# Kernel optimization log

Measured on AMD Instinct MI355X. Metric: run time of the kernel, lower is better.

## Reference

```python
import jax, jax.numpy as jnp
import numpy as np

B, H, S, DK, DV = 2, 16, 2048, 64, 64


def setup_inputs() -> dict:
    key = jax.random.key(0)
    kq, kk, kv = jax.random.split(key, 3)
    Q = jax.random.normal(kq, (B, H, S, DK), dtype=jnp.float32)
    K = jax.random.normal(kk, (B, H, S, DK), dtype=jnp.float32)
    V = jax.random.normal(kv, (B, H, S, DV), dtype=jnp.float32)
    # causal mask: True = masked (upper triangle), broadcast to [B,H,S,S]
    causal = jnp.triu(jnp.ones((S, S), dtype=bool), k=1)
    attn_mask = jnp.broadcast_to(causal, (B, H, S, S))
    return {"Q": Q, "K": K, "V": V, "attn_mask": attn_mask}


def reference(Q, K, V, attn_mask):
    d_k = Q.shape[-1]
    # scores: [B,H,len_q,len_k]
    scores = jnp.einsum('bhqd,bhkd->bhqk', Q, K) / jnp.sqrt(jnp.float32(d_k))
    scores = jnp.where(attn_mask, -jnp.inf, scores)
    attn = jax.nn.softmax(scores, axis=-1)
    # context: [B,H,len_q,d_v]
    context = jnp.einsum('bhqk,bhkv->bhqv', attn, V)
    return context
```

## Files before the change

kernel.cpp:

```cpp
#include <hip/hip_runtime.h>
#include <hip/hip_bf16.h>
#include <math.h>

#define S_LEN 2048
#define DKV 64
#define NBH 32
#define QBLK 128
#define NQB (S_LEN / QBLK)
#define NKT (S_LEN / 64)
#define TILE_SH 4096

typedef __attribute__((ext_vector_type(8))) short bf16x8;
typedef __attribute__((ext_vector_type(16))) float f32x16;
typedef __attribute__((ext_vector_type(4))) float f32x4;
typedef __attribute__((ext_vector_type(4))) unsigned uint4v;

__device__ __forceinline__ short f2bf(float f) {
    union { float f; unsigned u; } x; x.f = f;
    unsigned r = (x.u + 0x7FFFu + ((x.u >> 16) & 1u)) >> 16;
    return (short)r;
}

__device__ __forceinline__ unsigned cvtpk(float lo, float hi) {
    unsigned r;
    asm("v_cvt_pk_bf16_f32 %0, %1, %2" : "=v"(r) : "v"(lo), "v"(hi));
    return r;
}

#define GLOAD_LDS16(g, s)                                                        \
    __builtin_amdgcn_global_load_lds(                                            \
        (const __attribute__((address_space(1))) unsigned*)(g),                  \
        (__attribute__((address_space(3))) unsigned*)(s), 16, 0, 0)

__global__ __launch_bounds__(256)
void prep_kv(const float* __restrict__ K, const float* __restrict__ V,
             short* __restrict__ wsK, short* __restrict__ wsV) {
    const int tile = blockIdx.x, bh = blockIdx.y, tid = threadIdx.x;
    const float* Kp = K + ((size_t)bh * S_LEN + tile * 64) * DKV;
    const float* Vp = V + ((size_t)bh * S_LEN + tile * 64) * DKV;
    short* outK = wsK + ((size_t)bh * NKT + tile) * TILE_SH;
    short* outV = wsV + ((size_t)bh * NKT + tile) * TILE_SH;

    __shared__ short Klds[64 * 64];
    __shared__ short Vl[64 * 64];

#pragma unroll
    for (int i = 0; i < 2; ++i) {
        const int chunk = i * 256 + tid;
        const int row = chunk >> 3, c8 = chunk & 7;
        const float* ksrc = Kp + row * DKV + c8 * 8;
        float4 a = *(const float4*)ksrc, b = *(const float4*)(ksrc + 4);
        uint4v tw;
        tw[0] = cvtpk(a.x, a.y); tw[1] = cvtpk(a.z, a.w);
        tw[2] = cvtpk(b.x, b.y); tw[3] = cvtpk(b.z, b.w);
        const int sidxK = (((c8 >> 1) * 2 + (row >> 5)) * 64) |
                          (((c8 & 1) << 5) | (row & 31));
        *(uint4v*)&Klds[sidxK * 8] = tw;

        const float* vs = Vp + row * DKV + c8 * 8;
        float4 c = *(const float4*)vs, d = *(const float4*)(vs + 4);
        uint4v uw;
        uw[0] = cvtpk(c.x, c.y); uw[1] = cvtpk(c.z, c.w);
        uw[2] = cvtpk(d.x, d.y); uw[3] = cvtpk(d.z, d.w);
        *(uint4v*)&Vl[chunk * 8] = uw;
    }
    __syncthreads();

#pragma unroll
    for (int i = 0; i < 2; ++i) {
        const int s = i * 256 + tid;
        *(bf16x8*)(outK + s * 8) = *(const bf16x8*)&Klds[s * 8];
        const int group = s >> 6;
        const int cc = group >> 1, th = group & 1;
        const int lane = s & 63;
        const int hh = lane >> 5, r31 = lane & 31;
        const int vd = 32 * th + r31;
        const int key0 = 16 * cc + 8 * hh;
        bf16x8 t;
#pragma unroll
        for (int j = 0; j < 8; ++j) t[j] = Vl[(key0 + j) * 64 + vd];
        *(bf16x8*)(outV + s * 8) = t;
    }
}

__global__ __launch_bounds__(256, 2)
void attn_fwd(const float* __restrict__ Q, const short* __restrict__ wsK,
              const short* __restrict__ wsV, float* __restrict__ O) {
    const int tid = threadIdx.x;
    const int l   = tid & 63;
    const int w   = tid >> 6;
    const int qc  = w & 1;
    const int ks  = w >> 1;
    const int h   = l >> 5;
    const int q31 = l & 31;

    const int id  = blockIdx.x;
    const int bh  = ((id & 7) << 2) | ((id >> 3) & 3);
    const int r5  = (id >> 5) & 7;
    const int qb  = (id < 256) ? (15 - r5) : r5;

    __shared__ char smem[65536];
    char* kstaW = smem + w * 16384;
    float* combp = (float*)smem;

    const float SCALE = 0.125f * 1.4426950408889634f;
    const float M0 = 12.0f;

    bf16x8 qf[2][4];
#pragma unroll
    for (int sp = 0; sp < 2; ++sp) {
        const int qrow = qb * QBLK + qc * 64 + sp * 32 + q31;
        const float* qr = Q + ((size_t)bh * S_LEN + qrow) * DKV;
#pragma unroll
        for (int c = 0; c < 4; ++c) {
            const int k0 = c * 16 + h * 8;
            float4 f0 = *(const float4*)(qr + k0);
            float4 f1 = *(const float4*)(qr + k0 + 4);
            bf16x8 t;
            t[0] = f2bf(f0.x * SCALE); t[1] = f2bf(f0.y * SCALE);
            t[2] = f2bf(f0.z * SCALE); t[3] = f2bf(f0.w * SCALE);
            t[4] = f2bf(f1.x * SCALE); t[5] = f2bf(f1.y * SCALE);
            t[6] = f2bf(f1.z * SCALE); t[7] = f2bf(f1.w * SCALE);
            qf[sp][c] = t;
        }
    }

    const char* gK = (const char*)(wsK + (size_t)bh * NKT * TILE_SH);
    const char* gV = (const char*)(wsV + (size_t)bh * NKT * TILE_SH);
    const int lb = l * 16;

    float lsum[2] = {0.0f, 0.0f};
    f32x16 oacc[2][2];
#pragma unroll
    for (int sp = 0; sp < 2; ++sp)
#pragma unroll
        for (int vh = 0; vh < 2; ++vh)
#pragma unroll
            for (int r = 0; r < 16; ++r) oacc[sp][vh][r] = 0.0f;

    const int tmax = 2 * qb + qc;

    if (ks <= tmax) {
        const char* kT = gK + (size_t)ks * (TILE_SH * 2);
#pragma unroll
        for (int i = 0; i < 8; ++i)
            GLOAD_LDS16(kT + i * 1024 + lb, kstaW + i * 1024);
    }

    int cur = 0;
    for (int t = ks; t <= tmax; t += 2) {
        asm volatile("s_waitcnt vmcnt(0)" ::: "memory");
        bf16x8 kf[8];
#pragma unroll
        for (int i = 0; i < 8; ++i)
            kf[i] = *(const bf16x8*)(kstaW + cur * 8192 + i * 1024 + lb);

        if (t + 2 <= tmax) {
            const char* kT2 = gK + (size_t)(t + 2) * (TILE_SH * 2);
            char* nb = kstaW + (cur ^ 1) * 8192;
#pragma unroll
            for (int i = 0; i < 8; ++i)
                GLOAD_LDS16(kT2 + i * 1024 + lb, nb + i * 1024);
        }

        const char* vT = gV + (size_t)t * (TILE_SH * 2);
        bf16x8 vf[8];
#pragma unroll
        for (int i = 0; i < 8; ++i) vf[i] = *(const bf16x8*)(vT + i * 1024 + lb);

#pragma unroll
        for (int sp = 0; sp < 2; ++sp) {
            const int qrow = qb * QBLK + qc * 64 + sp * 32 + q31;

            f32x16 sacc[2];
#pragma unroll
            for (int th = 0; th < 2; ++th)
#pragma unroll
                for (int r = 0; r < 16; ++r) sacc[th][r] = 0.0f;

            __builtin_amdgcn_s_setprio(1);
#pragma unroll
            for (int c = 0; c < 4; ++c)
#pragma unroll
                for (int th = 0; th < 2; ++th)
                    sacc[th] = __builtin_amdgcn_mfma_f32_32x32x16_bf16(
                        kf[c * 2 + th], qf[sp][c], sacc[th], 0, 0, 0);
            __builtin_amdgcn_s_setprio(0);

            if (t == tmax) {
                const int kv0 = t * 64;
#pragma unroll
                for (int th = 0; th < 2; ++th)
#pragma unroll
                    for (int r = 0; r < 16; ++r) {
                        const int key_g = kv0 + 32 * th + (r & 3) + 8 * (r >> 2) + 4 * h;
                        if (key_g > qrow) sacc[th][r] = -3.0e38f;
                    }
            }

            float rs = 0.0f;
            __builtin_amdgcn_s_setprio(1);
#pragma unroll
            for (int c = 0; c < 4; ++c) {
                const int th = c >> 1, cc = c & 1;
                float p8[8];
#pragma unroll
                for (int j = 0; j < 8; ++j) {
                    p8[j] = __builtin_amdgcn_exp2f(sacc[th][8 * cc + j] - M0);
                    rs += p8[j];
                }
                const unsigned W00 = cvtpk(p8[0], p8[1]);
                const unsigned W01 = cvtpk(p8[2], p8[3]);
                const unsigned W10 = cvtpk(p8[4], p8[5]);
                const unsigned W11 = cvtpk(p8[6], p8[7]);
                const unsigned S0 = h ? W00 : W10;
                const unsigned S1 = h ? W01 : W11;
                const unsigned K0 = h ? W10 : W00;
                const unsigned K1 = h ? W11 : W01;
                const unsigned Y0 = __shfl_xor(S0, 32);
                const unsigned Y1 = __shfl_xor(S1, 32);
                uint4v pwv;
                pwv[0] = h ? Y0 : K0;
                pwv[1] = h ? Y1 : K1;
                pwv[2] = h ? K0 : Y0;
                pwv[3] = h ? K1 : Y1;
                const bf16x8 pa = __builtin_bit_cast(bf16x8, pwv);
#pragma unroll
                for (int vh = 0; vh < 2; ++vh)
                    oacc[sp][vh] = __builtin_amdgcn_mfma_f32_32x32x16_bf16(
                        vf[c * 2 + vh], pa, oacc[sp][vh], 0, 0, 0);
            }
            __builtin_amdgcn_s_setprio(0);

            rs += __shfl_xor(rs, 32);
            lsum[sp] += rs;
        }
        cur ^= 1;
    }

    __syncthreads();
    if (ks == 1) {
#pragma unroll
        for (int sp = 0; sp < 2; ++sp) {
            float* cp = combp + ((qc * 2 + sp) * 64 + l) * 34;
            cp[0] = lsum[sp];
#pragma unroll
            for (int vh = 0; vh < 2; ++vh)
#pragma unroll
                for (int r = 0; r < 16; ++r) cp[1 + vh * 16 + r] = oacc[sp][vh][r];
        }
    }
    __syncthreads();
    if (ks == 0) {
#pragma unroll
        for (int sp = 0; sp < 2; ++sp) {
            const float* cp = combp + ((qc * 2 + sp) * 64 + l) * 34;
            const float inv = 1.0f / (lsum[sp] + cp[0]);
            const int qrow = qb * QBLK + qc * 64 + sp * 32 + q31;
            float* Op = O + ((size_t)bh * S_LEN + qrow) * DKV;
#pragma unroll
            for (int vh = 0; vh < 2; ++vh) {
#pragma unroll
                for (int g2 = 0; g2 < 4; ++g2) {
                    f32x4 ov;
#pragma unroll
                    for (int d = 0; d < 4; ++d)
                        ov[d] = (oacc[sp][vh][4 * g2 + d] +
                                 cp[1 + vh * 16 + 4 * g2 + d]) * inv;
                    *(f32x4*)(Op + 32 * vh + 8 * g2 + 4 * h) = ov;
                }
            }
        }
    }
}

extern "C" void kernel_launch(void* const* d_in, const int* in_sizes, int n_in,
                              void* d_out, int out_size, void* d_ws, size_t ws_size,
                              hipStream_t stream) {
    const float* Q = (const float*)d_in[0];
    const float* K = (const float*)d_in[1];
    const float* V = (const float*)d_in[2];
    float* O = (float*)d_out;

    short* wsK = (short*)d_ws;
    short* wsV = wsK + (size_t)NBH * NKT * TILE_SH;

    dim3 gridp(NKT, NBH);
    prep_kv<<<gridp, 256, 0, stream>>>(K, V, wsK, wsV);
    attn_fwd<<<dim3(NQB * NBH), 256, 0, stream>>>(Q, wsK, wsV, O);
}
```

Before: 47.79 us.

## Halve query block to 64 rows and share K tiles across waves via LDS

Shrinks the query block per workgroup from 128 to 64 rows, so each wave handles one 32-row strip instead of two. Each K tile is now loaded cooperatively by a wave pair into shared LDS, with block-wide barriers each iteration. The LDS footprint is halved and launch bounds raised to 4 blocks per CU to increase occupancy and spread the causal workload over a larger grid. The cost is extra __syncthreads per tile and less reuse of each loaded K/V tile across query rows.

```diff
diff --git a/kernel.cpp b/kernel.cpp
--- a/kernel.cpp
+++ b/kernel.cpp
@@ -5,7 +5,7 @@
 #define S_LEN 2048
 #define DKV 64
 #define NBH 32
-#define QBLK 128
+#define QBLK 64
 #define NQB (S_LEN / QBLK)
 #define NKT (S_LEN / 64)
 #define TILE_SH 4096
@@ -83,33 +83,35 @@
     }
 }
 
-__global__ __launch_bounds__(256, 2)
+__global__ __launch_bounds__(256, 4)
 void attn_fwd(const float* __restrict__ Q, const short* __restrict__ wsK,
               const short* __restrict__ wsV, float* __restrict__ O) {
     const int tid = threadIdx.x;
     const int l   = tid & 63;
     const int w   = tid >> 6;
-    const int qc  = w & 1;
+    const int st  = w & 1;
     const int ks  = w >> 1;
     const int h   = l >> 5;
     const int q31 = l & 31;
 
-    const int id  = blockIdx.x;
-    const int bh  = ((id & 7) << 2) | ((id >> 3) & 3);
-    const int r5  = (id >> 5) & 7;
-    const int qb  = (id < 256) ? (15 - r5) : r5;
-
-    __shared__ char smem[65536];
-    char* kstaW = smem + w * 16384;
+    const int id = blockIdx.x;
+    const int bh = ((id & 7) << 2) | ((id >> 3) & 3);
+    const int r  = (id >> 5) & 7;
+    const int qt = id >> 8;
+    const int qb = (qt == 0) ? (31 - r) : (qt == 1) ? r
+                 : (qt == 2) ? (23 - r) : (8 + r);
+
+    __shared__ char smem[32768];
+    char* kls = smem + ks * 16384;
     float* combp = (float*)smem;
 
     const float SCALE = 0.125f * 1.4426950408889634f;
     const float M0 = 12.0f;
 
-    bf16x8 qf[2][4];
-#pragma unroll
-    for (int sp = 0; sp < 2; ++sp) {
-        const int qrow = qb * QBLK + qc * 64 + sp * 32 + q31;
+    const int qrow = qb * QBLK + st * 32 + q31;
+
+    bf16x8 qf[4];
+    {
         const float* qr = Q + ((size_t)bh * S_LEN + qrow) * DKV;
 #pragma unroll
         for (int c = 0; c < 4; ++c) {
@@ -121,7 +123,7 @@
             t[2] = f2bf(f0.z * SCALE); t[3] = f2bf(f0.w * SCALE);
             t[4] = f2bf(f1.x * SCALE); t[5] = f2bf(f1.y * SCALE);
             t[6] = f2bf(f1.z * SCALE); t[7] = f2bf(f1.w * SCALE);
-            qf[sp][c] = t;
+            qf[c] = t;
         }
     }
 
@@ -129,54 +131,50 @@
     const char* gV = (const char*)(wsV + (size_t)bh * NKT * TILE_SH);
     const int lb = l * 16;
 
-    float lsum[2] = {0.0f, 0.0f};
-    f32x16 oacc[2][2];
-#pragma unroll
-    for (int sp = 0; sp < 2; ++sp)
-#pragma unroll
-        for (int vh = 0; vh < 2; ++vh)
-#pragma unroll
-            for (int r = 0; r < 16; ++r) oacc[sp][vh][r] = 0.0f;
-
-    const int tmax = 2 * qb + qc;
-
-    if (ks <= tmax) {
-        const char* kT = gK + (size_t)ks * (TILE_SH * 2);
-#pragma unroll
-        for (int i = 0; i < 8; ++i)
-            GLOAD_LDS16(kT + i * 1024 + lb, kstaW + i * 1024);
-    }
-
+    float lsum = 0.0f;
+    f32x16 oacc[2];
+#pragma unroll
+    for (int vh = 0; vh < 2; ++vh)
+#pragma unroll
+        for (int rr = 0; rr < 16; ++rr) oacc[vh][rr] = 0.0f;
+
+    if (ks <= qb) {
+        const char* kT = gK + (size_t)ks * 8192;
+#pragma unroll
+        for (int i = 0; i < 4; ++i)
+            GLOAD_LDS16(kT + st * 4096 + i * 1024 + lb,
+                        kls + st * 4096 + i * 1024);
+    }
+
+    const int niter = qb / 2 + 1;
     int cur = 0;
-    for (int t = ks; t <= tmax; t += 2) {
+    for (int it = 0; it < niter; ++it) {
+        const int t = 2 * it + ks;
+        const bool active = (t <= qb);
+
         asm volatile("s_waitcnt vmcnt(0)" ::: "memory");
-        bf16x8 kf[8];
-#pragma unroll
-        for (int i = 0; i < 8; ++i)
-            kf[i] = *(const bf16x8*)(kstaW + cur * 8192 + i * 1024 + lb);
-
-        if (t + 2 <= tmax) {
-            const char* kT2 = gK + (size_t)(t + 2) * (TILE_SH * 2);
-            char* nb = kstaW + (cur ^ 1) * 8192;
+        __syncthreads();
+
+        if (active) {
+            bf16x8 kf[8];
 #pragma unroll
             for (int i = 0; i < 8; ++i)
-                GLOAD_LDS16(kT2 + i * 1024 + lb, nb + i * 1024);
-        }
-
-        const char* vT = gV + (size_t)t * (TILE_SH * 2);
-        bf16x8 vf[8];
-#pragma unroll
-        for (int i = 0; i < 8; ++i) vf[i] = *(const bf16x8*)(vT + i * 1024 + lb);
-
-#pragma unroll
-        for (int sp = 0; sp < 2; ++sp) {
-            const int qrow = qb * QBLK + qc * 64 + sp * 32 + q31;
+                kf[i] = *(const bf16x8*)(kls + cur * 8192 + i * 1024 + lb);
+
+            if (t + 2 <= qb) {
+                const char* kT2 = gK + (size_t)(t + 2) * 8192;
+                char* nb = kls + (cur ^ 1) * 8192;
+#pragma unroll
+                for (int i = 0; i < 4; ++i)
+                    GLOAD_LDS16(kT2 + st * 4096 + i * 1024 + lb,
+                                nb + st * 4096 + i * 1024);
+            }
 
             f32x16 sacc[2];
 #pragma unroll
             for (int th = 0; th < 2; ++th)
 #pragma unroll
-                for (int r = 0; r < 16; ++r) sacc[th][r] = 0.0f;
+                for (int rr = 0; rr < 16; ++rr) sacc[th][rr] = 0.0f;
 
             __builtin_amdgcn_s_setprio(1);
 #pragma unroll
@@ -184,17 +182,23 @@
 #pragma unroll
                 for (int th = 0; th < 2; ++th)
                     sacc[th] = __builtin_amdgcn_mfma_f32_32x32x16_bf16(
-                        kf[c * 2 + th], qf[sp][c], sacc[th], 0, 0, 0);
+                        kf[c * 2 + th], qf[c], sacc[th], 0, 0, 0);
             __builtin_amdgcn_s_setprio(0);
 
-            if (t == tmax) {
+            const char* vT = gV + (size_t)t * 8192;
+            bf16x8 vf[8];
+#pragma unroll
+            for (int i = 0; i < 8; ++i)
+                vf[i] = *(const bf16x8*)(vT + i * 1024 + lb);
+
+            if (t == qb) {
                 const int kv0 = t * 64;
 #pragma unroll
                 for (int th = 0; th < 2; ++th)
 #pragma unroll
-                    for (int r = 0; r < 16; ++r) {
-                        const int key_g = kv0 + 32 * th + (r & 3) + 8 * (r >> 2) + 4 * h;
-                        if (key_g > qrow) sacc[th][r] = -3.0e38f;
+                    for (int rr = 0; rr < 16; ++rr) {
+                        const int key_g = kv0 + 32 * th + (rr & 3) + 8 * (rr >> 2) + 4 * h;
+                        if (key_g > qrow) sacc[th][rr] = -3.0e38f;
                     }
             }
 
@@ -227,48 +231,41 @@
                 const bf16x8 pa = __builtin_bit_cast(bf16x8, pwv);
 #pragma unroll
                 for (int vh = 0; vh < 2; ++vh)
-                    oacc[sp][vh] = __builtin_amdgcn_mfma_f32_32x32x16_bf16(
-                        vf[c * 2 + vh], pa, oacc[sp][vh], 0, 0, 0);
+                    oacc[vh] = __builtin_amdgcn_mfma_f32_32x32x16_bf16(
+                        vf[c * 2 + vh], pa, oacc[vh], 0, 0, 0);
             }
             __builtin_amdgcn_s_setprio(0);
 
             rs += __shfl_xor(rs, 32);
-            lsum[sp] += rs;
+            lsum += rs;
         }
         cur ^= 1;
     }
 
     __syncthreads();
     if (ks == 1) {
-#pragma unroll
-        for (int sp = 0; sp < 2; ++sp) {
-            float* cp = combp + ((qc * 2 + sp) * 64 + l) * 34;
-            cp[0] = lsum[sp];
-#pragma unroll
-            for (int vh = 0; vh < 2; ++vh)
-#pragma unroll
-                for (int r = 0; r < 16; ++r) cp[1 + vh * 16 + r] = oacc[sp][vh][r];
-        }
+        float* cp = combp + (st * 64 + l) * 33;
+        cp[0] = lsum;
+#pragma unroll
+        for (int vh = 0; vh < 2; ++vh)
+#pragma unroll
+            for (int rr = 0; rr < 16; ++rr) cp[1 + vh * 16 + rr] = oacc[vh][rr];
     }
     __syncthreads();
     if (ks == 0) {
-#pragma unroll
-        for (int sp = 0; sp < 2; ++sp) {
-            const float* cp = combp + ((qc * 2 + sp) * 64 + l) * 34;
-            const float inv = 1.0f / (lsum[sp] + cp[0]);
-            const int qrow = qb * QBLK + qc * 64 + sp * 32 + q31;
-            float* Op = O + ((size_t)bh * S_LEN + qrow) * DKV;
-#pragma unroll
-            for (int vh = 0; vh < 2; ++vh) {
-#pragma unroll
-                for (int g2 = 0; g2 < 4; ++g2) {
-                    f32x4 ov;
-#pragma unroll
-                    for (int d = 0; d < 4; ++d)
-                        ov[d] = (oacc[sp][vh][4 * g2 + d] +
-                                 cp[1 + vh * 16 + 4 * g2 + d]) * inv;
-                    *(f32x4*)(Op + 32 * vh + 8 * g2 + 4 * h) = ov;
-                }
+        const float* cp = combp + (st * 64 + l) * 33;
+        const float inv = 1.0f / (lsum + cp[0]);
+        float* Op = O + ((size_t)bh * S_LEN + qrow) * DKV;
+#pragma unroll
+        for (int vh = 0; vh < 2; ++vh) {
+#pragma unroll
+            for (int g2 = 0; g2 < 4; ++g2) {
+                f32x4 ov;
+#pragma unroll
+                for (int d = 0; d < 4; ++d)
+                    ov[d] = (oacc[vh][4 * g2 + d] +
+                             cp[1 + vh * 16 + 4 * g2 + d]) * inv;
+                *(f32x4*)(Op + 32 * vh + 8 * g2 + 4 * h) = ov;
             }
         }
     }
```

Result: no change. 47.79 us (-0.0%).

## Fuse K/V bf16 conversion into attention kernel and drop prep pass

Applied to the files above, without the earlier changes.

Removes the separate prep_kv kernel that converted K and V to bf16 in a pre-swizzled workspace layout. The attention kernel now reads fp32 K and V straight from global memory and packs them into MFMA fragments in registers; V is gathered with per-element strided loads. This removes one launch and the workspace write and read round trip. In exchange it drops the LDS double-buffered K prefetch, doubles the bytes fetched per tile, and adds many more load and convert instructions in the inner loop.

```diff
diff --git a/kernel.cpp b/kernel.cpp
--- a/kernel.cpp
+++ b/kernel.cpp
@@ -8,7 +8,6 @@
 #define QBLK 128
 #define NQB (S_LEN / QBLK)
 #define NKT (S_LEN / 64)
-#define TILE_SH 4096
 
 typedef __attribute__((ext_vector_type(8))) short bf16x8;
 typedef __attribute__((ext_vector_type(16))) float f32x16;
@@ -27,65 +26,9 @@
     return r;
 }
 
-#define GLOAD_LDS16(g, s)                                                        \
-    __builtin_amdgcn_global_load_lds(                                            \
-        (const __attribute__((address_space(1))) unsigned*)(g),                  \
-        (__attribute__((address_space(3))) unsigned*)(s), 16, 0, 0)
-
-__global__ __launch_bounds__(256)
-void prep_kv(const float* __restrict__ K, const float* __restrict__ V,
-             short* __restrict__ wsK, short* __restrict__ wsV) {
-    const int tile = blockIdx.x, bh = blockIdx.y, tid = threadIdx.x;
-    const float* Kp = K + ((size_t)bh * S_LEN + tile * 64) * DKV;
-    const float* Vp = V + ((size_t)bh * S_LEN + tile * 64) * DKV;
-    short* outK = wsK + ((size_t)bh * NKT + tile) * TILE_SH;
-    short* outV = wsV + ((size_t)bh * NKT + tile) * TILE_SH;
-
-    __shared__ short Klds[64 * 64];
-    __shared__ short Vl[64 * 64];
-
-#pragma unroll
-    for (int i = 0; i < 2; ++i) {
-        const int chunk = i * 256 + tid;
-        const int row = chunk >> 3, c8 = chunk & 7;
-        const float* ksrc = Kp + row * DKV + c8 * 8;
-        float4 a = *(const float4*)ksrc, b = *(const float4*)(ksrc + 4);
-        uint4v tw;
-        tw[0] = cvtpk(a.x, a.y); tw[1] = cvtpk(a.z, a.w);
-        tw[2] = cvtpk(b.x, b.y); tw[3] = cvtpk(b.z, b.w);
-        const int sidxK = (((c8 >> 1) * 2 + (row >> 5)) * 64) |
-                          (((c8 & 1) << 5) | (row & 31));
-        *(uint4v*)&Klds[sidxK * 8] = tw;
-
-        const float* vs = Vp + row * DKV + c8 * 8;
-        float4 c = *(const float4*)vs, d = *(const float4*)(vs + 4);
-        uint4v uw;
-        uw[0] = cvtpk(c.x, c.y); uw[1] = cvtpk(c.z, c.w);
-        uw[2] = cvtpk(d.x, d.y); uw[3] = cvtpk(d.z, d.w);
-        *(uint4v*)&Vl[chunk * 8] = uw;
-    }
-    __syncthreads();
-
-#pragma unroll
-    for (int i = 0; i < 2; ++i) {
-        const int s = i * 256 + tid;
-        *(bf16x8*)(outK + s * 8) = *(const bf16x8*)&Klds[s * 8];
-        const int group = s >> 6;
-        const int cc = group >> 1, th = group & 1;
-        const int lane = s & 63;
-        const int hh = lane >> 5, r31 = lane & 31;
-        const int vd = 32 * th + r31;
-        const int key0 = 16 * cc + 8 * hh;
-        bf16x8 t;
-#pragma unroll
-        for (int j = 0; j < 8; ++j) t[j] = Vl[(key0 + j) * 64 + vd];
-        *(bf16x8*)(outV + s * 8) = t;
-    }
-}
-
 __global__ __launch_bounds__(256, 2)
-void attn_fwd(const float* __restrict__ Q, const short* __restrict__ wsK,
-              const short* __restrict__ wsV, float* __restrict__ O) {
+void attn_fwd(const float* __restrict__ Q, const float* __restrict__ K,
+              const float* __restrict__ V, float* __restrict__ O) {
     const int tid = threadIdx.x;
     const int l   = tid & 63;
     const int w   = tid >> 6;
@@ -99,9 +42,7 @@
     const int r5  = (id >> 5) & 7;
     const int qb  = (id < 256) ? (15 - r5) : r5;
 
-    __shared__ char smem[65536];
-    char* kstaW = smem + w * 16384;
-    float* combp = (float*)smem;
+    __shared__ float combp[2 * 2 * 64 * 34];
 
     const float SCALE = 0.125f * 1.4426950408889634f;
     const float M0 = 12.0f;
@@ -125,9 +66,8 @@
         }
     }
 
-    const char* gK = (const char*)(wsK + (size_t)bh * NKT * TILE_SH);
-    const char* gV = (const char*)(wsV + (size_t)bh * NKT * TILE_SH);
-    const int lb = l * 16;
+    const float* Kp = K + (size_t)bh * S_LEN * DKV;
+    const float* Vp = V + (size_t)bh * S_LEN * DKV;
 
     float lsum[2] = {0.0f, 0.0f};
     f32x16 oacc[2][2];
@@ -140,33 +80,50 @@
 
     const int tmax = 2 * qb + qc;
 
-    if (ks <= tmax) {
-        const char* kT = gK + (size_t)ks * (TILE_SH * 2);
-#pragma unroll
-        for (int i = 0; i < 8; ++i)
-            GLOAD_LDS16(kT + i * 1024 + lb, kstaW + i * 1024);
-    }
-
-    int cur = 0;
     for (int t = ks; t <= tmax; t += 2) {
-        asm volatile("s_waitcnt vmcnt(0)" ::: "memory");
+        const int kv0 = t * 64;
+
         bf16x8 kf[8];
 #pragma unroll
-        for (int i = 0; i < 8; ++i)
-            kf[i] = *(const bf16x8*)(kstaW + cur * 8192 + i * 1024 + lb);
-
-        if (t + 2 <= tmax) {
-            const char* kT2 = gK + (size_t)(t + 2) * (TILE_SH * 2);
-            char* nb = kstaW + (cur ^ 1) * 8192;
-#pragma unroll
-            for (int i = 0; i < 8; ++i)
-                GLOAD_LDS16(kT2 + i * 1024 + lb, nb + i * 1024);
-        }
-
-        const char* vT = gV + (size_t)t * (TILE_SH * 2);
+        for (int c = 0; c < 4; ++c) {
+#pragma unroll
+            for (int th = 0; th < 2; ++th) {
+                const float* kr = Kp + (size_t)(kv0 + 32 * th + q31) * DKV
+                                + c * 16 + h * 8;
+                float4 f0 = *(const float4*)kr;
+                float4 f1 = *(const float4*)(kr + 4);
+                uint4v wv;
+                wv[0] = cvtpk(f0.x, f0.y); wv[1] = cvtpk(f0.z, f0.w);
+                wv[2] = cvtpk(f1.x, f1.y); wv[3] = cvtpk(f1.z, f1.w);
+                kf[c * 2 + th] = __builtin_bit_cast(bf16x8, wv);
+            }
+        }
+
         bf16x8 vf[8];
 #pragma unroll
-        for (int i = 0; i < 8; ++i) vf[i] = *(const bf16x8*)(vT + i * 1024 + lb);
+        for (int half = 0; half < 2; ++half) {
+            float va[4][8];
+#pragma unroll
+            for (int fi = 0; fi < 4; ++fi) {
+                const int c  = (half * 4 + fi) >> 1;
+                const int vh = (half * 4 + fi) & 1;
+                const float* vb = Vp + (size_t)(kv0 + c * 16 + h * 8) * DKV
+                                + 32 * vh + q31;
+#pragma unroll
+                for (int j = 0; j < 8; ++j) va[fi][j] = vb[(size_t)j * DKV];
+            }
+#pragma unroll
+            for (int fi = 0; fi < 4; ++fi) {
+                const int c  = (half * 4 + fi) >> 1;
+                const int vh = (half * 4 + fi) & 1;
+                uint4v wv;
+                wv[0] = cvtpk(va[fi][0], va[fi][1]);
+                wv[1] = cvtpk(va[fi][2], va[fi][3]);
+                wv[2] = cvtpk(va[fi][4], va[fi][5]);
+                wv[3] = cvtpk(va[fi][6], va[fi][7]);
+                vf[c * 2 + vh] = __builtin_bit_cast(bf16x8, wv);
+            }
+        }
 
 #pragma unroll
         for (int sp = 0; sp < 2; ++sp) {
@@ -188,7 +145,6 @@
             __builtin_amdgcn_s_setprio(0);
 
             if (t == tmax) {
-                const int kv0 = t * 64;
 #pragma unroll
                 for (int th = 0; th < 2; ++th)
 #pragma unroll
@@ -235,10 +191,8 @@
             rs += __shfl_xor(rs, 32);
             lsum[sp] += rs;
         }
-        cur ^= 1;
-    }
-
-    __syncthreads();
+    }
+
     if (ks == 1) {
 #pragma unroll
         for (int sp = 0; sp < 2; ++sp) {
@@ -282,10 +236,5 @@
     const float* V = (const float*)d_in[2];
     float* O = (float*)d_out;
 
-    short* wsK = (short*)d_ws;
-    short* wsV = wsK + (size_t)NBH * NKT * TILE_SH;
-
-    dim3 gridp(NKT, NBH);
-    prep_kv<<<gridp, 256, 0, stream>>>(K, V, wsK, wsV);
-    attn_fwd<<<dim3(NQB * NBH), 256, 0, stream>>>(Q, wsK, wsV, O);
-}
+    attn_fwd<<<dim3(NQB * NBH), 256, 0, stream>>>(Q, K, V, O);
+}
```

Measured after the change: 78.35 us. +64.0%, slower.

## Fuse K/V bf16 prep into attention kernel with per-head atomic barrier

Applied to the files above, without the earlier changes.

Merges the separate K/V conversion kernel into the attention kernel. Each of the 512 blocks converts two K/V tiles for its head, then spins on a per-head atomic counter until all 16 blocks for that head have finished. The aim is to remove one kernel launch and the gap between the two kernels. In exchange it adds a memset launch and a spin-wait barrier, which relies on all 16 blocks of a head being co-resident and could deadlock if they are not.

```diff
diff --git a/kernel.cpp b/kernel.cpp
--- a/kernel.cpp
+++ b/kernel.cpp
@@ -32,74 +32,89 @@
         (const __attribute__((address_space(1))) unsigned*)(g),                  \
         (__attribute__((address_space(3))) unsigned*)(s), 16, 0, 0)
 
-__global__ __launch_bounds__(256)
-void prep_kv(const float* __restrict__ K, const float* __restrict__ V,
-             short* __restrict__ wsK, short* __restrict__ wsV) {
-    const int tile = blockIdx.x, bh = blockIdx.y, tid = threadIdx.x;
-    const float* Kp = K + ((size_t)bh * S_LEN + tile * 64) * DKV;
-    const float* Vp = V + ((size_t)bh * S_LEN + tile * 64) * DKV;
-    short* outK = wsK + ((size_t)bh * NKT + tile) * TILE_SH;
-    short* outV = wsV + ((size_t)bh * NKT + tile) * TILE_SH;
-
-    __shared__ short Klds[64 * 64];
-    __shared__ short Vl[64 * 64];
-
-#pragma unroll
-    for (int i = 0; i < 2; ++i) {
-        const int chunk = i * 256 + tid;
-        const int row = chunk >> 3, c8 = chunk & 7;
-        const float* ksrc = Kp + row * DKV + c8 * 8;
-        float4 a = *(const float4*)ksrc, b = *(const float4*)(ksrc + 4);
-        uint4v tw;
-        tw[0] = cvtpk(a.x, a.y); tw[1] = cvtpk(a.z, a.w);
-        tw[2] = cvtpk(b.x, b.y); tw[3] = cvtpk(b.z, b.w);
-        const int sidxK = (((c8 >> 1) * 2 + (row >> 5)) * 64) |
-                          (((c8 & 1) << 5) | (row & 31));
-        *(uint4v*)&Klds[sidxK * 8] = tw;
-
-        const float* vs = Vp + row * DKV + c8 * 8;
-        float4 c = *(const float4*)vs, d = *(const float4*)(vs + 4);
-        uint4v uw;
-        uw[0] = cvtpk(c.x, c.y); uw[1] = cvtpk(c.z, c.w);
-        uw[2] = cvtpk(d.x, d.y); uw[3] = cvtpk(d.z, d.w);
-        *(uint4v*)&Vl[chunk * 8] = uw;
+__global__ __launch_bounds__(256, 2)
+void fused_attn(const float* __restrict__ Q, const float* __restrict__ K,
+                const float* __restrict__ V, int* __restrict__ cnt,
+                short* __restrict__ wsK, short* __restrict__ wsV,
+                float* __restrict__ O) {
+    const int tid = threadIdx.x;
+    const int id  = blockIdx.x;
+    const int bh  = ((id & 7) << 2) | ((id >> 3) & 3);
+    const int jj  = id >> 5;
+
+    __shared__ char smem[65536];
+
+    {
+        short* Klds = (short*)smem;
+        short* Vl   = (short*)(smem + 8192);
+
+        for (int pp = 0; pp < 2; ++pp) {
+            const int tile = jj * 2 + pp;
+            const float* Kp = K + ((size_t)bh * S_LEN + tile * 64) * DKV;
+            const float* Vp = V + ((size_t)bh * S_LEN + tile * 64) * DKV;
+            short* outK = wsK + ((size_t)bh * NKT + tile) * TILE_SH;
+            short* outV = wsV + ((size_t)bh * NKT + tile) * TILE_SH;
+
+#pragma unroll
+            for (int i = 0; i < 2; ++i) {
+                const int chunk = i * 256 + tid;
+                const int row = chunk >> 3, c8 = chunk & 7;
+                const float* ksrc = Kp + row * DKV + c8 * 8;
+                float4 a = *(const float4*)ksrc, b = *(const float4*)(ksrc + 4);
+                uint4v tw;
+                tw[0] = cvtpk(a.x, a.y); tw[1] = cvtpk(a.z, a.w);
+                tw[2] = cvtpk(b.x, b.y); tw[3] = cvtpk(b.z, b.w);
+                const int sidxK = (((c8 >> 1) * 2 + (row >> 5)) * 64) |
+                                  (((c8 & 1) << 5) | (row & 31));
+                *(uint4v*)&Klds[sidxK * 8] = tw;
+
+                const float* vs = Vp + row * DKV + c8 * 8;
+                float4 c = *(const float4*)vs, d = *(const float4*)(vs + 4);
+                uint4v uw;
+                uw[0] = cvtpk(c.x, c.y); uw[1] = cvtpk(c.z, c.w);
+                uw[2] = cvtpk(d.x, d.y); uw[3] = cvtpk(d.z, d.w);
+                *(uint4v*)&Vl[chunk * 8] = uw;
+            }
+            __syncthreads();
+
+#pragma unroll
+            for (int i = 0; i < 2; ++i) {
+                const int s = i * 256 + tid;
+                *(bf16x8*)(outK + s * 8) = *(const bf16x8*)&Klds[s * 8];
+                const int group = s >> 6;
+                const int cc2 = group >> 1, th = group & 1;
+                const int lane = s & 63;
+                const int hh = lane >> 5, r31l = lane & 31;
+                const int vd = 32 * th + r31l;
+                const int key0 = 16 * cc2 + 8 * hh;
+                bf16x8 t;
+#pragma unroll
+                for (int j = 0; j < 8; ++j) t[j] = Vl[(key0 + j) * 64 + vd];
+                *(bf16x8*)(outV + s * 8) = t;
+            }
+            __syncthreads();
+        }
+    }
+
+    if (tid == 0) {
+        __threadfence();
+        atomicAdd(&cnt[bh], 1);
+        while (__hip_atomic_load(&cnt[bh], __ATOMIC_ACQUIRE,
+                                 __HIP_MEMORY_SCOPE_AGENT) < 16) {
+            __builtin_amdgcn_s_sleep(8);
+        }
     }
     __syncthreads();
 
-#pragma unroll
-    for (int i = 0; i < 2; ++i) {
-        const int s = i * 256 + tid;
-        *(bf16x8*)(outK + s * 8) = *(const bf16x8*)&Klds[s * 8];
-        const int group = s >> 6;
-        const int cc = group >> 1, th = group & 1;
-        const int lane = s & 63;
-        const int hh = lane >> 5, r31 = lane & 31;
-        const int vd = 32 * th + r31;
-        const int key0 = 16 * cc + 8 * hh;
-        bf16x8 t;
-#pragma unroll
-        for (int j = 0; j < 8; ++j) t[j] = Vl[(key0 + j) * 64 + vd];
-        *(bf16x8*)(outV + s * 8) = t;
-    }
-}
-
-__global__ __launch_bounds__(256, 2)
-void attn_fwd(const float* __restrict__ Q, const short* __restrict__ wsK,
-              const short* __restrict__ wsV, float* __restrict__ O) {
-    const int tid = threadIdx.x;
     const int l   = tid & 63;
     const int w   = tid >> 6;
     const int qc  = w & 1;
     const int ks  = w >> 1;
     const int h   = l >> 5;
     const int q31 = l & 31;
-
-    const int id  = blockIdx.x;
-    const int bh  = ((id & 7) << 2) | ((id >> 3) & 3);
     const int r5  = (id >> 5) & 7;
     const int qb  = (id < 256) ? (15 - r5) : r5;
 
-    __shared__ char smem[65536];
     char* kstaW = smem + w * 16384;
     float* combp = (float*)smem;
 
@@ -282,10 +297,10 @@
     const float* V = (const float*)d_in[2];
     float* O = (float*)d_out;
 
-    short* wsK = (short*)d_ws;
+    int*   cnt = (int*)d_ws;
+    short* wsK = (short*)((char*)d_ws + 1024);
     short* wsV = wsK + (size_t)NBH * NKT * TILE_SH;
 
-    dim3 gridp(NKT, NBH);
-    prep_kv<<<gridp, 256, 0, stream>>>(K, V, wsK, wsV);
-    attn_fwd<<<dim3(NQB * NBH), 256, 0, stream>>>(Q, wsK, wsV, O);
+    hipMemsetAsync(cnt, 0, NBH * sizeof(int), stream);
+    fused_attn<<<dim3(NQB * NBH), 256, 0, stream>>>(Q, K, V, cnt, wsK, wsV, O);
 }
```

After: 95.73 us. +100.3%, slower.
